# Kernel tuning notes

Hardware: AMD Instinct MI355X
Metric: run time of the kernel (lower is better)

The kernel has to match this reference:

```python
import jax, jax.numpy as jnp
import numpy as np

N_HEAD = 12
HEAD_SIZE = 64  # 768 / 12
SCALE = 1.0 / np.sqrt(HEAD_SIZE)


def setup_inputs() -> dict:
    key = jax.random.key(0)
    k1, k2, k3 = jax.random.split(key, 3)
    B, T, C = 8, 1024, 768
    x = jax.random.normal(k1, (B, T, C), dtype=jnp.float32)
    W_attn = jax.random.normal(k2, (C, 3 * C), dtype=jnp.float32) * 0.02
    b_attn = jax.random.normal(k3, (3 * C,), dtype=jnp.float32) * 0.02
    return {"x": x, "W_attn": W_attn, "b_attn": b_attn}


def reference(x, W_attn, b_attn):
    B, T, C = x.shape
    hs = C // N_HEAD
    qkv = x @ W_attn + b_attn                      # [B, T, 3C]
    q, k, v = jnp.split(qkv, 3, axis=-1)
    # [B, nh, T, hs]
    q = q.reshape(B, T, N_HEAD, hs).transpose(0, 2, 1, 3)
    k = k.reshape(B, T, N_HEAD, hs).transpose(0, 2, 1, 3)
    v = v.reshape(B, T, N_HEAD, hs).transpose(0, 2, 1, 3)
    scores = jnp.einsum('bhqd,bhkd->bhqk', q, k) * SCALE
    causal = jnp.tril(jnp.ones((T, T), dtype=bool))  # [T, T]
    # masked positions get -inf then relu -> 0; equivalent to where(mask, relu, 0)
    att = jnp.where(causal, jax.nn.relu(scores), 0.0)
    y = jnp.einsum('bhqk,bhkd->bhqd', att, v)      # [B, nh, T, hs]
    return y.transpose(0, 2, 1, 3).reshape(B, T, C)
```

## Files before the change

kernel.cpp:

```cpp
#include <hip/hip_runtime.h>
#include <stdint.h>

typedef __bf16 bf16;
typedef __attribute__((ext_vector_type(8))) __bf16 bf16x8;
typedef __attribute__((ext_vector_type(4))) __bf16 bf16x4;
typedef __attribute__((ext_vector_type(4))) float  f32x4;

#define ATT_SCALE 0.125f

__device__ __forceinline__ void async16(void* lds, const void* g) {
  __builtin_amdgcn_global_load_lds(
      (__attribute__((address_space(1))) void*)(void*)g,
      (__attribute__((address_space(3))) void*)lds,
      16, 0, 0);
}

__global__ void prep_kernel(const float* __restrict__ x, bf16* __restrict__ y,
                            const float* __restrict__ W, bf16* __restrict__ Wt) {
  __shared__ float tile[32][33];
  const int tid = threadIdx.x;
  if (blockIdx.x < 3072) {
    size_t i = ((size_t)blockIdx.x * 256 + tid) * 8;
    float4 a = *(const float4*)(x + i);
    float4 b = *(const float4*)(x + i + 4);
    bf16x8 o;
    o[0] = (bf16)a.x; o[1] = (bf16)a.y; o[2] = (bf16)a.z; o[3] = (bf16)a.w;
    o[4] = (bf16)b.x; o[5] = (bf16)b.y; o[6] = (bf16)b.z; o[7] = (bf16)b.w;
    *(bf16x8*)(y + i) = o;
  } else {
    const int bid = blockIdx.x - 3072;
    const int tx = tid & 31, ty = tid >> 5;
    const int n0 = (bid % 72) * 32, k0 = (bid / 72) * 32;
#pragma unroll
    for (int r = 0; r < 4; ++r)
      tile[ty + r * 8][tx] = W[(size_t)(k0 + ty + r * 8) * 2304 + n0 + tx];
    __syncthreads();
#pragma unroll
    for (int r = 0; r < 4; ++r)
      Wt[(size_t)(n0 + ty + r * 8) * 768 + k0 + tx] = (bf16)tile[tx][ty + r * 8];
  }
}

__global__ void qkv_gemm_kernel(const bf16* __restrict__ A, const bf16* __restrict__ Bw,
                                const float* __restrict__ bias,
                                bf16* __restrict__ Qo, bf16* __restrict__ Ko,
                                bf16* __restrict__ Vo) {
  __shared__ __align__(16) char lds[65536];

  const int tid  = threadIdx.x;
  const int wave = tid >> 6, lane = tid & 63;
  const int quad = lane >> 4, mn = lane & 15;
  const int wr = wave >> 1, wc = wave & 1;

  const int orig = blockIdx.y * 18 + blockIdx.x;
  const int swz  = (orig & 7) * 144 + (orig >> 3);
  const int m0 = (swz / 18) * 128;
  const int n0 = (swz % 18) * 128;

  f32x4 acc[4][4] = {};

  const int lrow = lane >> 3;
  const int cg   = (lane & 7) ^ lrow;

  auto stage = [&](int kt, char* buf) {
    char* Al = buf;
    char* Bl = buf + 16384;
#pragma unroll
    for (int u = 0; u < 4; ++u) {
      const int t   = wave * 4 + u;
      const int row = t * 8 + lrow;
      async16(Al + t * 1024 + lane * 16,
              A  + (size_t)(m0 + row) * 768 + kt + cg * 8);
      async16(Bl + t * 1024 + lane * 16,
              Bw + (size_t)(n0 + row) * 768 + kt + cg * 8);
    }
  };

#define SCHED0() __builtin_amdgcn_sched_barrier(0)

  stage(0, lds); SCHED0();

  for (int j = 0; j < 12; ++j) {
    asm volatile("s_waitcnt lgkmcnt(0)" ::: "memory"); SCHED0();
    __builtin_amdgcn_s_barrier(); SCHED0();
    if (j < 11) { stage((j + 1) * 64, lds + ((j + 1) & 1) * 32768); SCHED0(); }
    if (j < 11) { asm volatile("s_waitcnt vmcnt(8)" ::: "memory"); }
    else        { asm volatile("s_waitcnt vmcnt(0)" ::: "memory"); }
    SCHED0();
    __builtin_amdgcn_s_barrier(); SCHED0();

    char* Al = lds + (j & 1) * 32768;
    char* Bl = Al + 16384;

#pragma unroll
    for (int s = 0; s < 2; ++s) {
      bf16x8 af[4], bfr[4];
      const int csw = ((s * 4 + quad) ^ (mn & 7)) * 16;
#pragma unroll
      for (int i = 0; i < 4; ++i) {
        af[i]  = *(const bf16x8*)(Al + (wr * 64 + i * 16 + mn) * 128 + csw);
        bfr[i] = *(const bf16x8*)(Bl + (wc * 64 + i * 16 + mn) * 128 + csw);
      }
#pragma unroll
      for (int i = 0; i < 4; ++i)
#pragma unroll
        for (int jj = 0; jj < 4; ++jj)
          acc[i][jj] = __builtin_amdgcn_mfma_f32_16x16x32_bf16(af[i], bfr[jj], acc[i][jj], 0, 0, 0);
    }
  }

#undef SCHED0

  const int ng    = n0 + wc * 64;
  const int third = ng / 768;
  const int nmod  = ng % 768;
  const float sc  = (third == 0) ? ATT_SCALE : 1.0f;
#pragma unroll
  for (int ct = 0; ct < 4; ++ct) {
    int n = nmod + ct * 16 + mn;
    int h = n >> 6, d = n & 63;
    float bv = bias[third * 768 + n];
#pragma unroll
    for (int rt = 0; rt < 4; ++rt) {
      int m  = m0 + wr * 64 + rt * 16 + quad * 4;
      int b  = m >> 10, t0 = m & 1023;
      size_t bh = (size_t)b * 12 + h;
      if (third == 2) {
        bf16x4 pk;
#pragma unroll
        for (int r = 0; r < 4; ++r) pk[r] = (bf16)(acc[rt][ct][r] + bv);
        *(bf16x4*)(Vo + (bh * 64 + d) * 1024 + t0) = pk;
      } else {
        bf16* dst = (third == 0 ? Qo : Ko) + (bh * 1024 + t0) * 64 + d;
#pragma unroll
        for (int r = 0; r < 4; ++r) dst[(size_t)r * 64] = (bf16)((acc[rt][ct][r] + bv) * sc);
      }
    }
  }
}

__global__ __launch_bounds__(256, 3)
void attn_kernel(const bf16* __restrict__ Q, const bf16* __restrict__ K,
                 const bf16* __restrict__ Vt, float* __restrict__ out) {
  __shared__ __align__(16) char lds[49152];
  char* ldsS = lds + 32768;

  const int tid  = threadIdx.x;
  const int wave = tid >> 6, lane = tid & 63;
  const int quad = lane >> 4, mn = lane & 15;
  const int bh  = blockIdx.x;
  const int qta = blockIdx.y;
  const int qtb = 15 - qta;
  const int qa0 = qta * 64, qb0 = qtb * 64;

  const bf16* Qg  = Q  + (size_t)bh * 65536;
  const bf16* Kg0 = K  + (size_t)bh * 65536;
  const bf16* Vg0 = Vt + (size_t)bh * 65536;

#define SCHED0() __builtin_amdgcn_sched_barrier(0)

  bf16x8 qfA[2], qfB[2];
  {
    const bf16* ra = Qg + (size_t)(qa0 + wave * 16 + mn) * 64;
    qfA[0] = *(const bf16x8*)(ra + quad * 8);
    qfA[1] = *(const bf16x8*)(ra + 32 + quad * 8);
    const bf16* rb = Qg + (size_t)(qb0 + wave * 16 + mn) * 64;
    qfB[0] = *(const bf16x8*)(rb + quad * 8);
    qfB[1] = *(const bf16x8*)(rb + 32 + quad * 8);
  }
  SCHED0();

  f32x4 yA[4] = {}, yB[4] = {};

  const int lrow = lane >> 3;
  const int cg   = (lane & 7) ^ lrow;

  auto stageKV = [&](int j, char* buf) {
#pragma unroll
    for (int u2 = 0; u2 < 2; ++u2) {
      const int u   = wave * 2 + u2;
      const int row = u * 8 + lrow;
      async16(buf + u * 1024 + lane * 16,
              Kg0 + (size_t)(j * 64 + row) * 64 + cg * 8);
      async16(buf + 8192 + u * 1024 + lane * 16,
              Vg0 + (size_t)row * 1024 + j * 64 + cg * 8);
    }
  };

  const int srow = (wave * 16 + mn) * 128;

  stageKV(0, lds);  SCHED0();

  for (int j = 0; j <= qtb; ++j) {
    asm volatile("s_waitcnt lgkmcnt(0)" ::: "memory"); SCHED0();
    __builtin_amdgcn_s_barrier(); SCHED0();
    if (j < qtb) { stageKV(j + 1, lds + ((j + 1) & 1) * 16384); SCHED0(); }
    if (j < qtb) { asm volatile("s_waitcnt vmcnt(4)" ::: "memory"); }
    else         { asm volatile("s_waitcnt vmcnt(0)" ::: "memory"); }
    SCHED0();
    __builtin_amdgcn_s_barrier(); SCHED0();

    char* bK = lds + (j & 1) * 16384;
    char* bV = bK + 8192;

    bf16x8 kf[4][2], vf[4][2];
    const int sw = mn & 7;
#pragma unroll
    for (int ct = 0; ct < 4; ++ct) {
      const int ro = (ct * 16 + mn) * 128;
      kf[ct][0] = *(const bf16x8*)(bK + ro + ((quad)     ^ sw) * 16);
      kf[ct][1] = *(const bf16x8*)(bK + ro + ((4 + quad) ^ sw) * 16);
      vf[ct][0] = *(const bf16x8*)(bV + ro + ((quad)     ^ sw) * 16);
      vf[ct][1] = *(const bf16x8*)(bV + ro + ((4 + quad) ^ sw) * 16);
    }

    auto qk_half = [&](const bf16x8* qf, int half, int qrow, bool diag) {
#pragma unroll
      for (int ct = 0; ct < 4; ++ct) {
        f32x4 a = {};
        a = __builtin_amdgcn_mfma_f32_16x16x32_bf16(kf[ct][0], qf[0], a, 0, 0, 0);
        a = __builtin_amdgcn_mfma_f32_16x16x32_bf16(kf[ct][1], qf[1], a, 0, 0, 0);
        const int kkg = j * 64 + ct * 16 + quad * 4;
        bf16x4 pk;
#pragma unroll
        for (int r = 0; r < 4; ++r) {
          float v = a[r];
          v = v > 0.f ? v : 0.f;
          if (diag && kkg + r > qrow) v = 0.f;
          pk[r] = (bf16)v;
        }
        *(bf16x4*)(ldsS + half * 8192 + srow +
                   (((ct * 4 + quad) ^ (sw << 1)) & 15) * 8) = pk;
      }
    };
    auto sv_half = [&](f32x4* y, int half) {
#pragma unroll
      for (int kb = 0; kb < 2; ++kb) {
        bf16x8 sf = *(const bf16x8*)(ldsS + half * 8192 + srow +
                                     ((kb * 4 + quad) ^ sw) * 16);
#pragma unroll
        for (int ct = 0; ct < 4; ++ct)
          y[ct] = __builtin_amdgcn_mfma_f32_16x16x32_bf16(sf, vf[ct][kb], y[ct], 0, 0, 0);
      }
    };

    if (j <= qta) qk_half(qfA, 0, qa0 + wave * 16 + mn, j == qta);
    qk_half(qfB, 1, qb0 + wave * 16 + mn, j == qtb);
    if (j <= qta) sv_half(yA, 0);
    sv_half(yB, 1);
  }

#undef SCHED0

  const int b = bh / 12, h = bh % 12;
  {
    float* ob = out + ((size_t)b * 1024 + qa0 + wave * 16 + quad * 4) * 768 + h * 64;
#pragma unroll
    for (int ct = 0; ct < 4; ++ct)
#pragma unroll
      for (int r = 0; r < 4; ++r)
        ob[(size_t)r * 768 + ct * 16 + mn] = yA[ct][r];
  }
  {
    float* ob = out + ((size_t)b * 1024 + qb0 + wave * 16 + quad * 4) * 768 + h * 64;
#pragma unroll
    for (int ct = 0; ct < 4; ++ct)
#pragma unroll
      for (int r = 0; r < 4; ++r)
        ob[(size_t)r * 768 + ct * 16 + mn] = yB[ct][r];
  }
}

extern "C" void kernel_launch(void* const* d_in, const int* in_sizes, int n_in,
                              void* d_out, int out_size, void* d_ws, size_t ws_size,
                              hipStream_t stream) {
  const float* x    = (const float*)d_in[0];
  const float* W    = (const float*)d_in[1];
  const float* bias = (const float*)d_in[2];
  float* out = (float*)d_out;

  char* ws = (char*)d_ws;
  bf16* xb = (bf16*)(ws);
  bf16* Wt = (bf16*)(ws + 12582912);
  bf16* Qb = (bf16*)(ws + 16121856);
  bf16* Kb = (bf16*)(ws + 28704768);
  bf16* Vb = (bf16*)(ws + 41287680);

  prep_kernel<<<4800, 256, 0, stream>>>(x, xb, W, Wt);
  qkv_gemm_kernel<<<dim3(18, 64), 256, 0, stream>>>(xb, Wt, bias, Qb, Kb, Vb);
  attn_kernel<<<dim3(96, 8), 256, 0, stream>>>(Qb, Kb, Vb, out);
}
```

Before: 142.3 us.

## Load K/V fragments directly from global memory instead of double-buffered LDS staging

Removes the async global-to-LDS double-buffered staging of K and V tiles, along with its waitcnt and barrier synchronization. Each wave now reads its K and V MFMA fragments straight from global memory every iteration. This shrinks LDS use to just the score buffer and drops the block barriers, which may raise occupancy. The cost is that the four waves redundantly fetch the same K/V data through the cache with no prefetch overlap, so load latency is exposed.

```diff
diff --git a/kernel.cpp b/kernel.cpp
--- a/kernel.cpp
+++ b/kernel.cpp
@@ -142,8 +142,7 @@
 __global__ __launch_bounds__(256, 3)
 void attn_kernel(const bf16* __restrict__ Q, const bf16* __restrict__ K,
                  const bf16* __restrict__ Vt, float* __restrict__ out) {
-  __shared__ __align__(16) char lds[49152];
-  char* ldsS = lds + 32768;
+  __shared__ __align__(16) char ldsS[16384];
 
   const int tid  = threadIdx.x;
   const int wave = tid >> 6, lane = tid & 63;
@@ -156,8 +155,6 @@
   const bf16* Qg  = Q  + (size_t)bh * 65536;
   const bf16* Kg0 = K  + (size_t)bh * 65536;
   const bf16* Vg0 = Vt + (size_t)bh * 65536;
-
-#define SCHED0() __builtin_amdgcn_sched_barrier(0)
 
   bf16x8 qfA[2], qfB[2];
   {
@@ -168,50 +165,22 @@
     qfB[0] = *(const bf16x8*)(rb + quad * 8);
     qfB[1] = *(const bf16x8*)(rb + 32 + quad * 8);
   }
-  SCHED0();
 
   f32x4 yA[4] = {}, yB[4] = {};
 
-  const int lrow = lane >> 3;
-  const int cg   = (lane & 7) ^ lrow;
-
-  auto stageKV = [&](int j, char* buf) {
-#pragma unroll
-    for (int u2 = 0; u2 < 2; ++u2) {
-      const int u   = wave * 2 + u2;
-      const int row = u * 8 + lrow;
-      async16(buf + u * 1024 + lane * 16,
-              Kg0 + (size_t)(j * 64 + row) * 64 + cg * 8);
-      async16(buf + 8192 + u * 1024 + lane * 16,
-              Vg0 + (size_t)row * 1024 + j * 64 + cg * 8);
-    }
-  };
-
   const int srow = (wave * 16 + mn) * 128;
-
-  stageKV(0, lds);  SCHED0();
+  const int sw = mn & 7;
 
   for (int j = 0; j <= qtb; ++j) {
-    asm volatile("s_waitcnt lgkmcnt(0)" ::: "memory"); SCHED0();
-    __builtin_amdgcn_s_barrier(); SCHED0();
-    if (j < qtb) { stageKV(j + 1, lds + ((j + 1) & 1) * 16384); SCHED0(); }
-    if (j < qtb) { asm volatile("s_waitcnt vmcnt(4)" ::: "memory"); }
-    else         { asm volatile("s_waitcnt vmcnt(0)" ::: "memory"); }
-    SCHED0();
-    __builtin_amdgcn_s_barrier(); SCHED0();
-
-    char* bK = lds + (j & 1) * 16384;
-    char* bV = bK + 8192;
-
     bf16x8 kf[4][2], vf[4][2];
-    const int sw = mn & 7;
 #pragma unroll
     for (int ct = 0; ct < 4; ++ct) {
-      const int ro = (ct * 16 + mn) * 128;
-      kf[ct][0] = *(const bf16x8*)(bK + ro + ((quad)     ^ sw) * 16);
-      kf[ct][1] = *(const bf16x8*)(bK + ro + ((4 + quad) ^ sw) * 16);
-      vf[ct][0] = *(const bf16x8*)(bV + ro + ((quad)     ^ sw) * 16);
-      vf[ct][1] = *(const bf16x8*)(bV + ro + ((4 + quad) ^ sw) * 16);
+      const bf16* kr = Kg0 + (size_t)(j * 64 + ct * 16 + mn) * 64 + quad * 8;
+      kf[ct][0] = *(const bf16x8*)(kr);
+      kf[ct][1] = *(const bf16x8*)(kr + 32);
+      const bf16* vr = Vg0 + (size_t)(ct * 16 + mn) * 1024 + j * 64 + quad * 8;
+      vf[ct][0] = *(const bf16x8*)(vr);
+      vf[ct][1] = *(const bf16x8*)(vr + 32);
     }
 
     auto qk_half = [&](const bf16x8* qf, int half, int qrow, bool diag) {
@@ -250,8 +219,6 @@
     sv_half(yB, 1);
   }
 
-#undef SCHED0
-
   const int b = bh / 12, h = bh % 12;
   {
     float* ob = out + ((size_t)b * 1024 + qa0 + wave * 16 + quad * 4) * 768 + h * 64;
```

Result: slower. 192.7 us (+35.5%).
